# Kernel optimization log

Hardware: AMD Instinct MI355X
Metric: run time of the kernel (lower is better)

## Reference

```python
import jax, jax.numpy as jnp
import numpy as np

N = 4096          # nodes
E = 131072        # edges (avg degree 32)
D_IN = 128        # node_dim
H = 256           # hidden_dim
HEADS = 8
DH = H // HEADS


def setup_inputs() -> dict:
    key = jax.random.key(0)
    ks = jax.random.split(key, 24)
    w = lambda k, shape: (jax.random.normal(k, shape, dtype=jnp.float32) * 0.05)
    inp = {
        "x": jax.random.normal(ks[0], (N, D_IN), dtype=jnp.float32),
        "edge_index": jax.random.randint(ks[1], (2, E), 0, N, dtype=jnp.int32),
        # GCN conv weights (PyG GCNConv: out = aggr(norm * x @ W) + b)
        "W1": w(ks[2], (D_IN, H)), "b1": jnp.zeros((H,), jnp.float32),
        "W2": w(ks[3], (H, H)),    "b2": jnp.zeros((H,), jnp.float32),
        "W3": w(ks[4], (H, H)),    "b3": jnp.zeros((H,), jnp.float32),
        # nn.MultiheadAttention params (torch layout: y = x @ W.T + b)
        "in_w": w(ks[5], (3 * H, H)), "in_b": jnp.zeros((3 * H,), jnp.float32),
        "out_w": w(ks[6], (H, H)),    "out_b": jnp.zeros((H,), jnp.float32),
        # failure_predictor MLP: H -> H/2 -> 3
        "fp1_w": w(ks[7], (H // 2, H)), "fp1_b": jnp.zeros((H // 2,), jnp.float32),
        "fp2_w": w(ks[8], (3, H // 2)), "fp2_b": jnp.zeros((3,), jnp.float32),
        # pattern_detector MLP: H -> H/2 -> 10
        "pd1_w": w(ks[9], (H // 2, H)),  "pd1_b": jnp.zeros((H // 2,), jnp.float32),
        "pd2_w": w(ks[10], (10, H // 2)), "pd2_b": jnp.zeros((10,), jnp.float32),
    }
    return inp


def gcn_conv(x, src, dst, W, b):
    """PyG GCNConv with self-loops and symmetric normalization."""
    h = x @ W                                   # [N, H]
    deg = jnp.zeros((N,), x.dtype).at[dst].add(1.0) + 1.0   # +1 for self-loop
    dinv = jax.lax.rsqrt(deg)
    norm = dinv[src] * dinv[dst]                # [E]
    agg = jnp.zeros_like(h).at[dst].add(h[src] * norm[:, None])
    agg = agg + h * (1.0 / deg)[:, None]        # self-loop term: deg^-1/2 * deg^-1/2
    return agg + b


def mha(h, in_w, in_b, out_w, out_b):
    qkv = h @ in_w.T + in_b                     # [N, 3H]
    q, k, v = jnp.split(qkv, 3, axis=-1)
    q = q.reshape(N, HEADS, DH).transpose(1, 0, 2)   # [h, N, dh]
    k = k.reshape(N, HEADS, DH).transpose(1, 0, 2)
    v = v.reshape(N, HEADS, DH).transpose(1, 0, 2)
    scores = jnp.einsum("hnd,hmd->hnm", q, k) / np.sqrt(DH)
    attn = jax.nn.softmax(scores, axis=-1)
    o = jnp.einsum("hnm,hmd->hnd", attn, v)          # [h, N, dh]
    o = o.transpose(1, 0, 2).reshape(N, H)
    return o @ out_w.T + out_b


def reference(x, edge_index, W1, b1, W2, b2, W3, b3, in_w, in_b, out_w, out_b,
              fp1_w, fp1_b, fp2_w, fp2_b, pd1_w, pd1_b, pd2_w, pd2_b):
    src, dst = edge_index[0], edge_index[1]
    h = jax.nn.relu(gcn_conv(x, src, dst, W1, b1))   # dropout is identity in eval
    h = jax.nn.relu(gcn_conv(h, src, dst, W2, b2))
    h = gcn_conv(h, src, dst, W3, b3)
    h = h + mha(h, in_w, in_b, out_w, out_b)
    risk = jax.nn.softmax(jax.nn.relu(h @ fp1_w.T + fp1_b) @ fp2_w.T + fp2_b, axis=-1)
    patterns = jax.nn.sigmoid(jax.nn.relu(h @ pd1_w.T + pd1_b) @ pd2_w.T + pd2_b)
    return risk, patterns
```

## Files before the change

### kernel.cpp

```cpp
#include <hip/hip_runtime.h>
#include <math.h>

static constexpr int NNODE = 4096;
static constexpr int HDIM  = 256;
static constexpr int DIN   = 128;
static constexpr int HEADS = 8;
static constexpr int SPLIT = 4;

using short8 = __attribute__((ext_vector_type(8))) short;
using f32x4  = __attribute__((ext_vector_type(4))) float;

__device__ inline unsigned short bfr(float x) {
    union { float f; unsigned u; } v; v.f = x;
    unsigned r = v.u + 0x7FFFu + ((v.u >> 16) & 1u);
    return (unsigned short)(r >> 16);
}
__device__ inline float bf2f(unsigned short u) {
    union { unsigned u; float f; } v; v.u = (unsigned)u << 16; return v.f;
}
__device__ inline unsigned cvt_pk_bf16(float lo, float hi) {
    unsigned r;
    asm("v_cvt_pk_bf16_f32 %0, %1, %2" : "=v"(r) : "v"(lo), "v"(hi));
    return r;
}
__device__ inline float ex2(float x) {
    float r;
    asm("v_exp_f32 %0, %1" : "=v"(r) : "v"(x));
    return r;
}

static constexpr float QSCALE_LOG2 = 0.25503527f;

__global__ void k_deg(const int* __restrict__ ei, int* __restrict__ degi, int E) {
    int e = blockIdx.x * 256 + threadIdx.x;
    if (e < E) atomicAdd(&degi[ei[E + e]], 1);
}

__global__ __launch_bounds__(256) void k_scan_norm(const int* __restrict__ degi,
        int* __restrict__ off, int* __restrict__ cursor,
        float* __restrict__ dinv, float* __restrict__ invdeg) {
    __shared__ int partial[256];
    int t = threadIdx.x;
    int local[16];
    int s = 0;
    #pragma unroll
    for (int i = 0; i < 16; ++i) { local[i] = degi[t * 16 + i]; s += local[i]; }
    partial[t] = s;
    __syncthreads();
    #pragma unroll
    for (int d = 1; d < 256; d <<= 1) {
        int add = (t >= d) ? partial[t - d] : 0;
        __syncthreads();
        partial[t] += add;
        __syncthreads();
    }
    int b = partial[t] - s;
    #pragma unroll
    for (int i = 0; i < 16; ++i) {
        int n = t * 16 + i;
        off[n] = b; cursor[n] = b; b += local[i];
        float d = (float)local[i] + 1.0f;
        dinv[n]   = rsqrtf(d);
        invdeg[n] = 1.0f / d;
    }
}

__global__ void k_fill(const int* __restrict__ ei, int* __restrict__ cursor,
                       int* __restrict__ csr, int E) {
    int e = blockIdx.x * 256 + threadIdx.x;
    if (e < E) {
        int d = ei[E + e];
        int p = atomicAdd(&cursor[d], 1);
        csr[p] = ei[e];
    }
}

__global__ __launch_bounds__(256) void k_prep(
        const float* __restrict__ W1, const float* __restrict__ W2,
        const float* __restrict__ W3, const float* __restrict__ in_w,
        const float* __restrict__ outw, const float* __restrict__ fp1w,
        const float* __restrict__ pd1w, const float* __restrict__ fp1b,
        const float* __restrict__ pd1b, const float* __restrict__ x,
        unsigned short* __restrict__ W1t, unsigned short* __restrict__ W2t,
        unsigned short* __restrict__ W3t, unsigned short* __restrict__ in_wb,
        unsigned short* __restrict__ outwb, unsigned short* __restrict__ wcatb,
        float* __restrict__ bcat, unsigned short* __restrict__ xb) {
    int idx = blockIdx.x * 256 + threadIdx.x;
    if (idx < 32768) {
        int c = idx >> 7, k = idx & 127;
        W1t[idx] = bfr(W1[(size_t)k * 256 + c]);
    } else if (idx < 98304) {
        int j = idx - 32768; int c = j >> 8, k = j & 255;
        W2t[j] = bfr(W2[(size_t)k * 256 + c]);
    } else if (idx < 163840) {
        int j = idx - 98304; int c = j >> 8, k = j & 255;
        W3t[j] = bfr(W3[(size_t)k * 256 + c]);
    } else if (idx < 360448) {
        int j = idx - 163840;
        in_wb[j] = bfr(in_w[j]);
    } else if (idx < 425984) {
        int j = idx - 360448;
        outwb[j] = bfr(outw[j]);
    } else if (idx < 491520) {
        int j = idx - 425984;
        int row = j >> 8, k = j & 255;
        wcatb[j] = bfr(row < 128 ? fp1w[(size_t)row * 256 + k]
                                 : pd1w[(size_t)(row - 128) * 256 + k]);
        if (j < 256) bcat[j] = (j < 128) ? fp1b[j] : pd1b[j - 128];
    } else if (idx < 557056) {
        int i = (idx - 491520) * 8;
        float4 a = *(const float4*)&x[i];
        float4 b = *(const float4*)&x[i + 4];
        short8 o;
        o[0]=(short)bfr(a.x); o[1]=(short)bfr(a.y); o[2]=(short)bfr(a.z); o[3]=(short)bfr(a.w);
        o[4]=(short)bfr(b.x); o[5]=(short)bfr(b.y); o[6]=(short)bfr(b.z); o[7]=(short)bfr(b.w);
        *(short8*)&xb[i] = o;
    }
}

template<int K, int EPI, bool BIAS, bool ADD>
__global__ __launch_bounds__(256) void k_bgemm(
        const unsigned short* __restrict__ A, const unsigned short* __restrict__ B,
        const float* __restrict__ bias, const float* __restrict__ addsrc,
        void* __restrict__ P0, void* __restrict__ P1, void* __restrict__ P2,
        int Nout) {
    const int lane = threadIdx.x & 63, wave = threadIdx.x >> 6;
    const int ql = lane & 15, g = lane >> 4;
    const int m0w = blockIdx.y * 64 + wave * 16;
    const int n0 = blockIdx.x * 32;
    const unsigned short* ap = A + (size_t)(m0w + ql) * K + g * 8;
    const unsigned short* bp = B + (size_t)(n0 + ql) * K + g * 8;

    f32x4 acc[2] = {{0,0,0,0},{0,0,0,0}};
    #pragma unroll
    for (int k0 = 0; k0 < K; k0 += 32) {
        short8 a = *(const short8*)(ap + k0);
        #pragma unroll
        for (int nt = 0; nt < 2; ++nt) {
            short8 b = *(const short8*)(bp + (size_t)nt * 16 * K + k0);
            acc[nt] = __builtin_amdgcn_mfma_f32_16x16x32_bf16(a, b, acc[nt], 0, 0, 0);
        }
    }
    #pragma unroll
    for (int nt = 0; nt < 2; ++nt) {
        const int col = n0 + nt * 16 + ql;
        const float bv = BIAS ? bias[col] : 0.f;
        if (EPI == 2) {
            const int sec = col >> 8, cc = col & 255;
            const int head = cc >> 5, dh = cc & 31;
            if (sec == 2) {
                unsigned short* dst = (unsigned short*)P2
                    + ((size_t)head * 32 + dh) * NNODE + m0w + g * 4;
                uint2 pk;
                pk.x = cvt_pk_bf16(acc[nt][0] + bv, acc[nt][1] + bv);
                pk.y = cvt_pk_bf16(acc[nt][2] + bv, acc[nt][3] + bv);
                *(uint2*)dst = pk;
            } else {
                unsigned short* dst = (unsigned short*)(sec == 0 ? P0 : P1);
                const float sc = (sec == 0) ? QSCALE_LOG2 : 1.0f;
                #pragma unroll
                for (int i = 0; i < 4; ++i) {
                    int row = m0w + g * 4 + i;
                    dst[((size_t)head * NNODE + row) * 32 + dh] = bfr((acc[nt][i] + bv) * sc);
                }
            }
        } else if (EPI == 1) {
            unsigned short* Cb = (unsigned short*)P0;
            #pragma unroll
            for (int i = 0; i < 4; ++i) {
                int row = m0w + g * 4 + i;
                float v = acc[nt][i] + bv;
                if (ADD) v += addsrc[(size_t)row * Nout + col];
                Cb[(size_t)row * Nout + col] = bfr(v);
            }
        } else {
            float* Cf = (float*)P0;
            #pragma unroll
            for (int i = 0; i < 4; ++i) {
                int row = m0w + g * 4 + i;
                float v = acc[nt][i] + bv;
                if (ADD) v += addsrc[(size_t)row * Nout + col];
                Cf[(size_t)row * Nout + col] = v;
            }
        }
    }
}

template<int MODE>
__global__ __launch_bounds__(256) void k_gather(const unsigned short* __restrict__ hW,
        const int* __restrict__ csr, const int* __restrict__ off,
        const int* __restrict__ degi, const float* __restrict__ dinv,
        const float* __restrict__ invdeg, const float* __restrict__ bias,
        float* __restrict__ aggf, unsigned short* __restrict__ aggb) {
    const int n = blockIdx.x;
    const int c = threadIdx.x;
    const int start = off[n];
    const int cnt = degi[n];
    __shared__ int   sidx[64];
    __shared__ float swht[64];
    float acc = 0.f;
    for (int k0 = 0; k0 < cnt; k0 += 64) {
        __syncthreads();
        if (c < 64 && k0 + c < cnt) {
            int s = csr[start + k0 + c];
            sidx[c] = s;
            swht[c] = dinv[s];
        }
        __syncthreads();
        int lim = min(64, cnt - k0);
        for (int k = 0; k < lim; ++k)
            acc += bf2f(hW[(size_t)sidx[k] * HDIM + c]) * swht[k];
    }
    float val = acc * dinv[n] + bf2f(hW[(size_t)n * HDIM + c]) * invdeg[n] + bias[c];
    if (MODE == 0) {
        aggb[(size_t)n * HDIM + c] = bfr(fmaxf(val, 0.f));
    } else {
        aggf[(size_t)n * HDIM + c] = val;
        aggb[(size_t)n * HDIM + c] = bfr(val);
    }
}

__global__ __launch_bounds__(256, 4) void k_attn_mfma(const unsigned short* __restrict__ qh,
        const unsigned short* __restrict__ kh, const unsigned short* __restrict__ vt,
        unsigned short* __restrict__ po, float* __restrict__ pm, float* __restrict__ pl) {
    const int bid = blockIdx.x;
    const int hd = bid & 7;
    const int z  = (bid >> 3) & (SPLIT - 1);
    const int qb = bid >> 5;
    const int tid = threadIdx.x;
    const int wave = tid >> 6, lane = tid & 63;
    const int ql = lane & 15, g = lane >> 4;

    __shared__ unsigned short Vt[2][32 * 72];
    __shared__ unsigned short Plds[4][32 * 72];

    const unsigned short* khh = kh + (size_t)hd * NNODE * 32;
    const unsigned short* vtt = vt + (size_t)hd * 32 * NNODE;
    const int row0 = qb * 128 + wave * 32 + ql;
    const int row1 = row0 + 16;
    short8 qf0 = *(const short8*)(qh + ((size_t)hd * NNODE + row0) * 32 + g * 8);
    short8 qf1 = *(const short8*)(qh + ((size_t)hd * NNODE + row1) * 32 + g * 8);

    f32x4 oa00 = {0,0,0,0}, oa01 = {0,0,0,0};
    f32x4 oa10 = {0,0,0,0}, oa11 = {0,0,0,0};
    float m0 = -INFINITY, l0 = 0.f, m1 = -INFINITY, l1 = 0.f;

    const int sdh = tid >> 3, sch = (tid & 7) * 8;
    const unsigned short* vsrc = vtt + (size_t)sdh * NNODE + sch;
    const unsigned short* kbase = khh + (size_t)ql * 32 + g * 8;
    const int TPS = NNODE / 64 / SPLIT;
    const int t0 = z * TPS;

    {
        short8 vv = *(const short8*)(vsrc + t0 * 64);
        *(short8*)&Vt[0][sdh * 72 + sch] = vv;
    }
    __syncthreads();
    int cur = 0;

    for (int kt = t0; kt < t0 + TPS; ++kt) {
        short8 vv;
        const bool pref = (kt + 1 < t0 + TPS);
        if (pref) vv = *(const short8*)(vsrc + (kt + 1) * 64);

        f32x4 st0[4], st1[4];
        __builtin_amdgcn_s_setprio(1);
        #pragma unroll
        for (int t = 0; t < 4; ++t) {
            short8 kf = *(const short8*)(kbase + ((size_t)kt * 64 + t * 16) * 32);
            st0[t] = __builtin_amdgcn_mfma_f32_16x16x32_bf16(kf, qf0, (f32x4){0,0,0,0}, 0, 0, 0);
            st1[t] = __builtin_amdgcn_mfma_f32_16x16x32_bf16(kf, qf1, (f32x4){0,0,0,0}, 0, 0, 0);
        }
        __builtin_amdgcn_s_setprio(0);

        {
            float mloc = -INFINITY;
            #pragma unroll
            for (int t = 0; t < 4; ++t)
                mloc = fmaxf(mloc, fmaxf(fmaxf(st0[t][0], st0[t][1]), fmaxf(st0[t][2], st0[t][3])));
            mloc = fmaxf(mloc, __shfl_xor(mloc, 16));
            mloc = fmaxf(mloc, __shfl_xor(mloc, 32));
            if (!__all(mloc <= m0 + 8.f)) {
                float mnew = fmaxf(m0, mloc);
                float corr = ex2(m0 - mnew);
                l0 *= corr; oa00 *= corr; oa01 *= corr; m0 = mnew;
            }
            float ll = 0.f;
            #pragma unroll
            for (int t = 0; t < 4; ++t) {
                float p0 = ex2(st0[t][0] - m0);
                float p1 = ex2(st0[t][1] - m0);
                float p2 = ex2(st0[t][2] - m0);
                float p3 = ex2(st0[t][3] - m0);
                ll += (p0 + p1) + (p2 + p3);
                uint2 w2; w2.x = cvt_pk_bf16(p0, p1); w2.y = cvt_pk_bf16(p2, p3);
                *(uint2*)&Plds[wave][ql * 72 + t * 16 + g * 4] = w2;
            }
            ll += __shfl_xor(ll, 16);
            ll += __shfl_xor(ll, 32);
            l0 += ll;
        }
        {
            float mloc = -INFINITY;
            #pragma unroll
            for (int t = 0; t < 4; ++t)
                mloc = fmaxf(mloc, fmaxf(fmaxf(st1[t][0], st1[t][1]), fmaxf(st1[t][2], st1[t][3])));
            mloc = fmaxf(mloc, __shfl_xor(mloc, 16));
            mloc = fmaxf(mloc, __shfl_xor(mloc, 32));
            if (!__all(mloc <= m1 + 8.f)) {
                float mnew = fmaxf(m1, mloc);
                float corr = ex2(m1 - mnew);
                l1 *= corr; oa10 *= corr; oa11 *= corr; m1 = mnew;
            }
            float ll = 0.f;
            #pragma unroll
            for (int t = 0; t < 4; ++t) {
                float p0 = ex2(st1[t][0] - m1);
                float p1 = ex2(st1[t][1] - m1);
                float p2 = ex2(st1[t][2] - m1);
                float p3 = ex2(st1[t][3] - m1);
                ll += (p0 + p1) + (p2 + p3);
                uint2 w2; w2.x = cvt_pk_bf16(p0, p1); w2.y = cvt_pk_bf16(p2, p3);
                *(uint2*)&Plds[wave][(16 + ql) * 72 + t * 16 + g * 4] = w2;
            }
            ll += __shfl_xor(ll, 16);
            ll += __shfl_xor(ll, 32);
            l1 += ll;
        }

        if (pref) *(short8*)&Vt[cur ^ 1][sdh * 72 + sch] = vv;

        __builtin_amdgcn_s_setprio(1);
        #pragma unroll
        for (int c = 0; c < 2; ++c) {
            short8 v0  = *(const short8*)&Vt[cur][ql * 72 + c * 32 + g * 8];
            short8 v1  = *(const short8*)&Vt[cur][(16 + ql) * 72 + c * 32 + g * 8];
            short8 pf0 = *(const short8*)&Plds[wave][ql * 72 + c * 32 + g * 8];
            short8 pf1 = *(const short8*)&Plds[wave][(16 + ql) * 72 + c * 32 + g * 8];
            oa00 = __builtin_amdgcn_mfma_f32_16x16x32_bf16(v0, pf0, oa00, 0, 0, 0);
            oa01 = __builtin_amdgcn_mfma_f32_16x16x32_bf16(v1, pf0, oa01, 0, 0, 0);
            oa10 = __builtin_amdgcn_mfma_f32_16x16x32_bf16(v0, pf1, oa10, 0, 0, 0);
            oa11 = __builtin_amdgcn_mfma_f32_16x16x32_bf16(v1, pf1, oa11, 0, 0, 0);
        }
        __builtin_amdgcn_s_setprio(0);
        __syncthreads();
        cur ^= 1;
    }

    const size_t pidx0 = ((size_t)hd * NNODE + row0) * SPLIT + z;
    const size_t pidx1 = ((size_t)hd * NNODE + row1) * SPLIT + z;
    unsigned short* pp0 = po + pidx0 * 32;
    unsigned short* pp1 = po + pidx1 * 32;
    uint2 r;
    r.x = cvt_pk_bf16(oa00[0], oa00[1]); r.y = cvt_pk_bf16(oa00[2], oa00[3]);
    *(uint2*)&pp0[g * 4] = r;
    r.x = cvt_pk_bf16(oa01[0], oa01[1]); r.y = cvt_pk_bf16(oa01[2], oa01[3]);
    *(uint2*)&pp0[16 + g * 4] = r;
    r.x = cvt_pk_bf16(oa10[0], oa10[1]); r.y = cvt_pk_bf16(oa10[2], oa10[3]);
    *(uint2*)&pp1[g * 4] = r;
    r.x = cvt_pk_bf16(oa11[0], oa11[1]); r.y = cvt_pk_bf16(oa11[2], oa11[3]);
    *(uint2*)&pp1[16 + g * 4] = r;
    if (g == 0) { pm[pidx0] = m0; pl[pidx0] = l0; pm[pidx1] = m1; pl[pidx1] = l1; }
}

__global__ __launch_bounds__(256) void k_attn_merge(const unsigned short* __restrict__ po,
        const float* __restrict__ pm, const float* __restrict__ pl,
        unsigned short* __restrict__ ob) {
    int idx = blockIdx.x * 256 + threadIdx.x;
    int row = idx >> 8, c = idx & 255;
    int hd = c >> 5, dh = c & 31;
    size_t b4 = ((size_t)hd * NNODE + row) * SPLIT;
    float m0 = pm[b4+0], m1 = pm[b4+1], m2 = pm[b4+2], m3 = pm[b4+3];
    float M = fmaxf(fmaxf(m0, m1), fmaxf(m2, m3));
    float w0 = ex2(m0 - M), w1 = ex2(m1 - M);
    float w2 = ex2(m2 - M), w3 = ex2(m3 - M);
    float L = pl[b4]*w0 + pl[b4+1]*w1 + pl[b4+2]*w2 + pl[b4+3]*w3;
    float v = bf2f(po[(b4+0)*32 + dh])*w0 + bf2f(po[(b4+1)*32 + dh])*w1
            + bf2f(po[(b4+2)*32 + dh])*w2 + bf2f(po[(b4+3)*32 + dh])*w3;
    ob[idx] = bfr(v / L);
}

__global__ __launch_bounds__(256) void k_heads2(const float* __restrict__ th,
        const float* __restrict__ fp2w, const float* __restrict__ fp2b,
        const float* __restrict__ pd2w, const float* __restrict__ pd2b,
        float* __restrict__ out) {
    const int wave = threadIdx.x >> 6, lane = threadIdx.x & 63;
    const int n = blockIdx.x * 4 + wave;
    const int half = lane >> 5;
    const int li = lane & 31;
    float4 h4 = *(const float4*)&th[(size_t)n * HDIM + half * 128 + li * 4];
    h4.x = fmaxf(h4.x, 0.f); h4.y = fmaxf(h4.y, 0.f);
    h4.z = fmaxf(h4.z, 0.f); h4.w = fmaxf(h4.w, 0.f);
    float lf[3];
    float lp[10];
    #pragma unroll
    for (int j = 0; j < 10; ++j) {
        float partial = 0.f;
        if (half == 0) {
            if (j < 3) {
                float4 wv = *(const float4*)&fp2w[j * 128 + li * 4];
                partial = h4.x*wv.x + h4.y*wv.y + h4.z*wv.z + h4.w*wv.w;
            }
        } else {
            float4 wv = *(const float4*)&pd2w[j * 128 + li * 4];
            partial = h4.x*wv.x + h4.y*wv.y + h4.z*wv.z + h4.w*wv.w;
        }
        #pragma unroll
        for (int d = 1; d < 32; d <<= 1) partial += __shfl_xor(partial, d);
        if (j < 3) lf[j] = partial;
        lp[j] = partial;
    }
    if (lane == 0) {
        float l0 = lf[0] + fp2b[0], l1 = lf[1] + fp2b[1], l2 = lf[2] + fp2b[2];
        float mx = fmaxf(l0, fmaxf(l1, l2));
        float e0 = __expf(l0 - mx), e1 = __expf(l1 - mx), e2 = __expf(l2 - mx);
        float inv = 1.f / (e0 + e1 + e2);
        out[(size_t)n * 3 + 0] = e0 * inv;
        out[(size_t)n * 3 + 1] = e1 * inv;
        out[(size_t)n * 3 + 2] = e2 * inv;
    } else if (lane == 32) {
        #pragma unroll
        for (int j = 0; j < 10; ++j)
            out[(size_t)NNODE * 3 + (size_t)n * 10 + j] =
                1.f / (1.f + __expf(-(lp[j] + pd2b[j])));
    }
}

extern "C" void kernel_launch(void* const* d_in, const int* in_sizes, int n_in,
                              void* d_out, int out_size, void* d_ws, size_t ws_size,
                              hipStream_t stream) {
    const float* x    = (const float*)d_in[0];
    const int*   ei   = (const int*)  d_in[1];
    const float* W1   = (const float*)d_in[2];
    const float* b1   = (const float*)d_in[3];
    const float* W2   = (const float*)d_in[4];
    const float* b2   = (const float*)d_in[5];
    const float* W3   = (const float*)d_in[6];
    const float* b3   = (const float*)d_in[7];
    const float* in_w = (const float*)d_in[8];
    const float* in_b = (const float*)d_in[9];
    const float* outw = (const float*)d_in[10];
    const float* outb = (const float*)d_in[11];
    const float* fp1w = (const float*)d_in[12];
    const float* fp1b = (const float*)d_in[13];
    const float* fp2w = (const float*)d_in[14];
    const float* fp2b = (const float*)d_in[15];
    const float* pd1w = (const float*)d_in[16];
    const float* pd1b = (const float*)d_in[17];
    const float* pd2w = (const float*)d_in[18];
    const float* pd2b = (const float*)d_in[19];
    float* out = (float*)d_out;

    const int E = in_sizes[1] / 2;

    char* w = (char*)d_ws;
    auto alloc = [&](size_t bytes) {
        char* p = w; w += (bytes + 255) & ~(size_t)255; return p;
    };
    int*   degi   = (int*)alloc(NNODE * 4);
    int*   off    = (int*)alloc(NNODE * 4);
    int*   cursor = (int*)alloc(NNODE * 4);
    int*   csr    = (int*)alloc((size_t)E * 4);
    float* dinv   = (float*)alloc(NNODE * 4);
    float* invdeg = (float*)alloc(NNODE * 4);
    unsigned short* W1t   = (unsigned short*)alloc(256 * 128 * 2);
    unsigned short* W2t   = (unsigned short*)alloc(256 * 256 * 2);
    unsigned short* W3t   = (unsigned short*)alloc(256 * 256 * 2);
    unsigned short* in_wb = (unsigned short*)alloc(768 * 256 * 2);
    unsigned short* outwb = (unsigned short*)alloc(256 * 256 * 2);
    unsigned short* wcatb = (unsigned short*)alloc(256 * 256 * 2);
    float* bcat  = (float*)alloc(256 * 4);
    unsigned short* xb    = (unsigned short*)alloc((size_t)NNODE * DIN * 2);
    float* bufA  = (float*)alloc((size_t)NNODE * HDIM * 4);
    unsigned short* bufAb = (unsigned short*)alloc((size_t)NNODE * HDIM * 2);
    unsigned short* aggb1 = (unsigned short*)alloc((size_t)NNODE * HDIM * 2);
    unsigned short* aggb2 = (unsigned short*)alloc((size_t)NNODE * HDIM * 2);
    float* hf    = (float*)alloc((size_t)NNODE * HDIM * 4);
    unsigned short* hb    = (unsigned short*)alloc((size_t)NNODE * HDIM * 2);
    unsigned short* qh    = (unsigned short*)alloc((size_t)HEADS * NNODE * 32 * 2);
    unsigned short* kh    = (unsigned short*)alloc((size_t)HEADS * NNODE * 32 * 2);
    unsigned short* vt    = (unsigned short*)alloc((size_t)HEADS * 32 * NNODE * 2);
    unsigned short* po    = (unsigned short*)alloc((size_t)HEADS * NNODE * SPLIT * 32 * 2);
    float* pm    = (float*)alloc((size_t)HEADS * NNODE * SPLIT * 4);
    float* pl    = (float*)alloc((size_t)HEADS * NNODE * SPLIT * 4);
    unsigned short* ob    = (unsigned short*)alloc((size_t)NNODE * HDIM * 2);
    unsigned short* hfinb = (unsigned short*)alloc((size_t)NNODE * HDIM * 2);

    hipMemsetAsync(degi, 0, NNODE * sizeof(int), stream);
    k_deg<<<(E + 255) / 256, 256, 0, stream>>>(ei, degi, E);
    k_scan_norm<<<1, 256, 0, stream>>>(degi, off, cursor, dinv, invdeg);
    k_fill<<<(E + 255) / 256, 256, 0, stream>>>(ei, cursor, csr, E);
    k_prep<<<2176, 256, 0, stream>>>(W1, W2, W3, in_w, outw, fp1w, pd1w, fp1b, pd1b, x,
                                     W1t, W2t, W3t, in_wb, outwb, wcatb, bcat, xb);

    dim3 g256(HDIM / 32, NNODE / 64);
    dim3 g768(768 / 32, NNODE / 64);

    k_bgemm<DIN, 1, false, false><<<g256, 256, 0, stream>>>(xb, W1t, nullptr, nullptr, bufAb, nullptr, nullptr, HDIM);
    k_gather<0><<<NNODE, 256, 0, stream>>>(bufAb, csr, off, degi, dinv, invdeg, b1, nullptr, aggb1);
    k_bgemm<HDIM, 1, false, false><<<g256, 256, 0, stream>>>(aggb1, W2t, nullptr, nullptr, bufAb, nullptr, nullptr, HDIM);
    k_gather<0><<<NNODE, 256, 0, stream>>>(bufAb, csr, off, degi, dinv, invdeg, b2, nullptr, aggb2);
    k_bgemm<HDIM, 1, false, false><<<g256, 256, 0, stream>>>(aggb2, W3t, nullptr, nullptr, bufAb, nullptr, nullptr, HDIM);
    k_gather<1><<<NNODE, 256, 0, stream>>>(bufAb, csr, off, degi, dinv, invdeg, b3, hf, hb);

    k_bgemm<HDIM, 2, true, false><<<g768, 256, 0, stream>>>(hb, in_wb, in_b, nullptr, qh, kh, vt, 768);
    k_attn_mfma<<<HEADS * SPLIT * (NNODE / 128), 256, 0, stream>>>(qh, kh, vt, po, pm, pl);
    k_attn_merge<<<(NNODE * HDIM) / 256, 256, 0, stream>>>(po, pm, pl, ob);
    k_bgemm<HDIM, 1, true, true><<<g256, 256, 0, stream>>>(ob, outwb, outb, hf, hfinb, nullptr, nullptr, HDIM);

    k_bgemm<HDIM, 0, true, false><<<g256, 256, 0, stream>>>(hfinb, wcatb, bcat, nullptr, bufA, nullptr, nullptr, HDIM);
    k_heads2<<<NNODE / 4, 256, 0, stream>>>(bufA, fp2w, fp2b, pd2w, pd2b, out);
}
```

Before: 183.7 us.

## Double attention KV split, halve P scratch, raise occupancy, unroll gather accumulators

Attention now splits the key range 8 ways instead of 4. Each wave handles its two 16-row query halves one after the other (score MFMA, softmax, then PV), which shrinks the P staging buffer in LDS and lowers register pressure. Launch bounds ask for 8 blocks per CU. The merge kernel is generalised to loop over SPLIT partials, and the GCN gather loop now uses four independent accumulators to expose more memory-level parallelism. The costs are more partial outputs to write and merge, and the second half reuses the same P buffer, which adds ordering dependencies within each wave.

```diff
diff --git a/kernel.cpp b/kernel.cpp
--- a/kernel.cpp
+++ b/kernel.cpp
@@ -5,7 +5,7 @@
 static constexpr int HDIM  = 256;
 static constexpr int DIN   = 128;
 static constexpr int HEADS = 8;
-static constexpr int SPLIT = 4;
+static constexpr int SPLIT = 8;
 
 using short8 = __attribute__((ext_vector_type(8))) short;
 using f32x4  = __attribute__((ext_vector_type(4))) float;
@@ -198,7 +198,7 @@
     const int cnt = degi[n];
     __shared__ int   sidx[64];
     __shared__ float swht[64];
-    float acc = 0.f;
+    float a0 = 0.f, a1 = 0.f, a2 = 0.f, a3 = 0.f;
     for (int k0 = 0; k0 < cnt; k0 += 64) {
         __syncthreads();
         if (c < 64 && k0 + c < cnt) {
@@ -208,9 +208,17 @@
         }
         __syncthreads();
         int lim = min(64, cnt - k0);
-        for (int k = 0; k < lim; ++k)
-            acc += bf2f(hW[(size_t)sidx[k] * HDIM + c]) * swht[k];
-    }
+        int k = 0;
+        for (; k + 4 <= lim; k += 4) {
+            a0 += bf2f(hW[(size_t)sidx[k+0] * HDIM + c]) * swht[k+0];
+            a1 += bf2f(hW[(size_t)sidx[k+1] * HDIM + c]) * swht[k+1];
+            a2 += bf2f(hW[(size_t)sidx[k+2] * HDIM + c]) * swht[k+2];
+            a3 += bf2f(hW[(size_t)sidx[k+3] * HDIM + c]) * swht[k+3];
+        }
+        for (; k < lim; ++k)
+            a0 += bf2f(hW[(size_t)sidx[k] * HDIM + c]) * swht[k];
+    }
+    float acc = (a0 + a1) + (a2 + a3);
     float val = acc * dinv[n] + bf2f(hW[(size_t)n * HDIM + c]) * invdeg[n] + bias[c];
     if (MODE == 0) {
         aggb[(size_t)n * HDIM + c] = bfr(fmaxf(val, 0.f));
@@ -220,19 +228,62 @@
     }
 }
 
-__global__ __launch_bounds__(256, 4) void k_attn_mfma(const unsigned short* __restrict__ qh,
+__device__ inline void softmax_half(f32x4 st[4], float& m, float& l,
+        f32x4& oaA, f32x4& oaB, unsigned short* prow, int g) {
+    float mloc = -INFINITY;
+    #pragma unroll
+    for (int t = 0; t < 4; ++t)
+        mloc = fmaxf(mloc, fmaxf(fmaxf(st[t][0], st[t][1]), fmaxf(st[t][2], st[t][3])));
+    mloc = fmaxf(mloc, __shfl_xor(mloc, 16));
+    mloc = fmaxf(mloc, __shfl_xor(mloc, 32));
+    if (!__all(mloc <= m + 8.f)) {
+        float mnew = fmaxf(m, mloc);
+        float corr = ex2(m - mnew);
+        l *= corr; oaA *= corr; oaB *= corr; m = mnew;
+    }
+    float ll = 0.f;
+    #pragma unroll
+    for (int t = 0; t < 4; ++t) {
+        float p0 = ex2(st[t][0] - m);
+        float p1 = ex2(st[t][1] - m);
+        float p2 = ex2(st[t][2] - m);
+        float p3 = ex2(st[t][3] - m);
+        ll += (p0 + p1) + (p2 + p3);
+        uint2 w2; w2.x = cvt_pk_bf16(p0, p1); w2.y = cvt_pk_bf16(p2, p3);
+        *(uint2*)&prow[t * 16 + g * 4] = w2;
+    }
+    ll += __shfl_xor(ll, 16);
+    ll += __shfl_xor(ll, 32);
+    l += ll;
+}
+
+__device__ inline void pv_half(const unsigned short* Vc, const unsigned short* prow,
+        f32x4& oaA, f32x4& oaB, int ql, int g) {
+    __builtin_amdgcn_s_setprio(1);
+    #pragma unroll
+    for (int c = 0; c < 2; ++c) {
+        short8 pf = *(const short8*)&prow[c * 32 + g * 8];
+        short8 v0 = *(const short8*)&Vc[ql * 72 + c * 32 + g * 8];
+        short8 v1 = *(const short8*)&Vc[(16 + ql) * 72 + c * 32 + g * 8];
+        oaA = __builtin_amdgcn_mfma_f32_16x16x32_bf16(v0, pf, oaA, 0, 0, 0);
+        oaB = __builtin_amdgcn_mfma_f32_16x16x32_bf16(v1, pf, oaB, 0, 0, 0);
+    }
+    __builtin_amdgcn_s_setprio(0);
+}
+
+__global__ __launch_bounds__(256, 8) void k_attn_mfma(const unsigned short* __restrict__ qh,
         const unsigned short* __restrict__ kh, const unsigned short* __restrict__ vt,
         unsigned short* __restrict__ po, float* __restrict__ pm, float* __restrict__ pl) {
     const int bid = blockIdx.x;
     const int hd = bid & 7;
     const int z  = (bid >> 3) & (SPLIT - 1);
-    const int qb = bid >> 5;
+    const int qb = bid >> 6;
     const int tid = threadIdx.x;
     const int wave = tid >> 6, lane = tid & 63;
     const int ql = lane & 15, g = lane >> 4;
 
     __shared__ unsigned short Vt[2][32 * 72];
-    __shared__ unsigned short Plds[4][32 * 72];
+    __shared__ unsigned short Plds[4][16 * 72];
 
     const unsigned short* khh = kh + (size_t)hd * NNODE * 32;
     const unsigned short* vtt = vt + (size_t)hd * 32 * NNODE;
@@ -248,6 +299,7 @@
     const int sdh = tid >> 3, sch = (tid & 7) * 8;
     const unsigned short* vsrc = vtt + (size_t)sdh * NNODE + sch;
     const unsigned short* kbase = khh + (size_t)ql * 32 + g * 8;
+    unsigned short* prow = &Plds[wave][ql * 72];
     const int TPS = NNODE / 64 / SPLIT;
     const int t0 = z * TPS;
 
@@ -263,86 +315,34 @@
         const bool pref = (kt + 1 < t0 + TPS);
         if (pref) vv = *(const short8*)(vsrc + (kt + 1) * 64);
 
-        f32x4 st0[4], st1[4];
-        __builtin_amdgcn_s_setprio(1);
-        #pragma unroll
-        for (int t = 0; t < 4; ++t) {
-            short8 kf = *(const short8*)(kbase + ((size_t)kt * 64 + t * 16) * 32);
-            st0[t] = __builtin_amdgcn_mfma_f32_16x16x32_bf16(kf, qf0, (f32x4){0,0,0,0}, 0, 0, 0);
-            st1[t] = __builtin_amdgcn_mfma_f32_16x16x32_bf16(kf, qf1, (f32x4){0,0,0,0}, 0, 0, 0);
-        }
-        __builtin_amdgcn_s_setprio(0);
-
         {
-            float mloc = -INFINITY;
-            #pragma unroll
-            for (int t = 0; t < 4; ++t)
-                mloc = fmaxf(mloc, fmaxf(fmaxf(st0[t][0], st0[t][1]), fmaxf(st0[t][2], st0[t][3])));
-            mloc = fmaxf(mloc, __shfl_xor(mloc, 16));
-            mloc = fmaxf(mloc, __shfl_xor(mloc, 32));
-            if (!__all(mloc <= m0 + 8.f)) {
-                float mnew = fmaxf(m0, mloc);
-                float corr = ex2(m0 - mnew);
-                l0 *= corr; oa00 *= corr; oa01 *= corr; m0 = mnew;
-            }
-            float ll = 0.f;
+            f32x4 st[4];
+            __builtin_amdgcn_s_setprio(1);
             #pragma unroll
             for (int t = 0; t < 4; ++t) {
-                float p0 = ex2(st0[t][0] - m0);
-                float p1 = ex2(st0[t][1] - m0);
-                float p2 = ex2(st0[t][2] - m0);
-                float p3 = ex2(st0[t][3] - m0);
-                ll += (p0 + p1) + (p2 + p3);
-                uint2 w2; w2.x = cvt_pk_bf16(p0, p1); w2.y = cvt_pk_bf16(p2, p3);
-                *(uint2*)&Plds[wave][ql * 72 + t * 16 + g * 4] = w2;
+                short8 kf = *(const short8*)(kbase + ((size_t)kt * 64 + t * 16) * 32);
+                st[t] = __builtin_amdgcn_mfma_f32_16x16x32_bf16(kf, qf0, (f32x4){0,0,0,0}, 0, 0, 0);
             }
-            ll += __shfl_xor(ll, 16);
-            ll += __shfl_xor(ll, 32);
-            l0 += ll;
-        }
+            __builtin_amdgcn_s_setprio(0);
+            softmax_half(st, m0, l0, oa00, oa01, prow, g);
+            pv_half(Vt[cur], prow, oa00, oa01, ql, g);
+        }
+
+        if (pref) *(short8*)&Vt[cur ^ 1][sdh * 72 + sch] = vv;
+
         {
-            float mloc = -INFINITY;
-            #pragma unroll
-            for (int t = 0; t < 4; ++t)
-                mloc = fmaxf(mloc, fmaxf(fmaxf(st1[t][0], st1[t][1]), fmaxf(st1[t][2], st1[t][3])));
-            mloc = fmaxf(mloc, __shfl_xor(mloc, 16));
-            mloc = fmaxf(mloc, __shfl_xor(mloc, 32));
-            if (!__all(mloc <= m1 + 8.f)) {
-                float mnew = fmaxf(m1, mloc);
-                float corr = ex2(m1 - mnew);
-                l1 *= corr; oa10 *= corr; oa11 *= corr; m1 = mnew;
-            }
-            float ll = 0.f;
+            f32x4 st[4];
+            __builtin_amdgcn_s_setprio(1);
             #pragma unroll
             for (int t = 0; t < 4; ++t) {
-                float p0 = ex2(st1[t][0] - m1);
-                float p1 = ex2(st1[t][1] - m1);
-                float p2 = ex2(st1[t][2] - m1);
-                float p3 = ex2(st1[t][3] - m1);
-                ll += (p0 + p1) + (p2 + p3);
-                uint2 w2; w2.x = cvt_pk_bf16(p0, p1); w2.y = cvt_pk_bf16(p2, p3);
-                *(uint2*)&Plds[wave][(16 + ql) * 72 + t * 16 + g * 4] = w2;
+                short8 kf = *(const short8*)(kbase + ((size_t)kt * 64 + t * 16) * 32);
+                st[t] = __builtin_amdgcn_mfma_f32_16x16x32_bf16(kf, qf1, (f32x4){0,0,0,0}, 0, 0, 0);
             }
-            ll += __shfl_xor(ll, 16);
-            ll += __shfl_xor(ll, 32);
-            l1 += ll;
-        }
-
-        if (pref) *(short8*)&Vt[cur ^ 1][sdh * 72 + sch] = vv;
-
-        __builtin_amdgcn_s_setprio(1);
-        #pragma unroll
-        for (int c = 0; c < 2; ++c) {
-            short8 v0  = *(const short8*)&Vt[cur][ql * 72 + c * 32 + g * 8];
-            short8 v1  = *(const short8*)&Vt[cur][(16 + ql) * 72 + c * 32 + g * 8];
-            short8 pf0 = *(const short8*)&Plds[wave][ql * 72 + c * 32 + g * 8];
-            short8 pf1 = *(const short8*)&Plds[wave][(16 + ql) * 72 + c * 32 + g * 8];
-            oa00 = __builtin_amdgcn_mfma_f32_16x16x32_bf16(v0, pf0, oa00, 0, 0, 0);
-            oa01 = __builtin_amdgcn_mfma_f32_16x16x32_bf16(v1, pf0, oa01, 0, 0, 0);
-            oa10 = __builtin_amdgcn_mfma_f32_16x16x32_bf16(v0, pf1, oa10, 0, 0, 0);
-            oa11 = __builtin_amdgcn_mfma_f32_16x16x32_bf16(v1, pf1, oa11, 0, 0, 0);
-        }
-        __builtin_amdgcn_s_setprio(0);
+            __builtin_amdgcn_s_setprio(0);
+            softmax_half(st, m1, l1, oa10, oa11, prow, g);
+            pv_half(Vt[cur], prow, oa10, oa11, ql, g);
+        }
+
         __syncthreads();
         cur ^= 1;
     }
@@ -369,14 +369,18 @@
     int idx = blockIdx.x * 256 + threadIdx.x;
     int row = idx >> 8, c = idx & 255;
     int hd = c >> 5, dh = c & 31;
-    size_t b4 = ((size_t)hd * NNODE + row) * SPLIT;
-    float m0 = pm[b4+0], m1 = pm[b4+1], m2 = pm[b4+2], m3 = pm[b4+3];
-    float M = fmaxf(fmaxf(m0, m1), fmaxf(m2, m3));
-    float w0 = ex2(m0 - M), w1 = ex2(m1 - M);
-    float w2 = ex2(m2 - M), w3 = ex2(m3 - M);
-    float L = pl[b4]*w0 + pl[b4+1]*w1 + pl[b4+2]*w2 + pl[b4+3]*w3;
-    float v = bf2f(po[(b4+0)*32 + dh])*w0 + bf2f(po[(b4+1)*32 + dh])*w1
-            + bf2f(po[(b4+2)*32 + dh])*w2 + bf2f(po[(b4+3)*32 + dh])*w3;
+    size_t b8 = ((size_t)hd * NNODE + row) * SPLIT;
+    float mm[SPLIT];
+    float M = -INFINITY;
+    #pragma unroll
+    for (int i = 0; i < SPLIT; ++i) { mm[i] = pm[b8 + i]; M = fmaxf(M, mm[i]); }
+    float L = 0.f, v = 0.f;
+    #pragma unroll
+    for (int i = 0; i < SPLIT; ++i) {
+        float w = ex2(mm[i] - M);
+        L += pl[b8 + i] * w;
+        v += bf2f(po[(b8 + i) * 32 + dh]) * w;
+    }
     ob[idx] = bfr(v / L);
 }
 
```

Measured after the change: 210.8 us. +14.7%, slower.
